# Performance work log

Measured on AMD Instinct MI355X. Metric: run time of the kernel, lower is better.

Reference implementation:

```python
import jax, jax.numpy as jnp
import numpy as np


def setup_inputs() -> dict:
    key = jax.random.key(0)
    k1, k2, k3, k4, k5 = jax.random.split(key, 5)
    B, C, H, W = 8, 256, 64, 64
    Cp = C // 8  # query/key channels
    x = jax.random.normal(k1, (B, C, H, W), dtype=jnp.float32)
    # 1x1 conv weights (bias=False in the module), spectral norm treated as a fixed weight scale
    Wq = jax.random.normal(k2, (Cp, C), dtype=jnp.float32) * 0.05
    Wk = jax.random.normal(k3, (Cp, C), dtype=jnp.float32) * 0.05
    Wv = jax.random.normal(k4, (C, C), dtype=jnp.float32) * 0.05
    gamma = jax.random.normal(k5, (1,), dtype=jnp.float32)
    return {"x": x, "Wq": Wq, "Wk": Wk, "Wv": Wv, "gamma": gamma}


def reference(x, Wq, Wk, Wv, gamma):
    B, C, H, W = x.shape
    xf = x.reshape(B, C, H * W)  # (B, C, N)
    # ConvLayer = 1x1 conv (no bias) followed by ReLU
    f = jax.nn.relu(jnp.einsum('oc,bcn->bon', Wq, xf))  # (B, C', N)
    g = jax.nn.relu(jnp.einsum('oc,bcn->bon', Wk, xf))  # (B, C', N)
    h = jax.nn.relu(jnp.einsum('oc,bcn->bon', Wv, xf))  # (B, C, N)
    # beta = softmax(f^T g, dim=1): normalize over the FIRST N axis (faithful to source)
    scores = jnp.einsum('bcn,bcm->bnm', f, g)  # (B, N, N)
    beta = jax.nn.softmax(scores, axis=1)
    o = gamma * jnp.einsum('bcn,bnm->bcm', h, beta) + xf  # (B, C, N)
    return o.reshape(B, C, H, W)
```

## Files before the change

kernel.cpp:

```cpp
#include <hip/hip_runtime.h>


typedef __attribute__((ext_vector_type(8))) short bf16x8;
typedef __attribute__((ext_vector_type(4))) float f32x4;
typedef __attribute__((ext_vector_type(4))) unsigned short us4;

#define LOG2E 1.44269504088896f

static __device__ __forceinline__ unsigned short f2bf(float x) {
    union { float f; unsigned u; } v; v.f = x;
    unsigned r = v.u + 0x7FFFu + ((v.u >> 16) & 1u);
    return (unsigned short)(r >> 16);
}
static __device__ __forceinline__ float bf2f(unsigned short u) {
    union { unsigned u; float f; } v; v.u = ((unsigned)u) << 16;
    return v.f;
}

__global__ __launch_bounds__(256) void wconv_kernel(
    const float* __restrict__ Wq, const float* __restrict__ Wk,
    const float* __restrict__ Wv, unsigned short* __restrict__ wq,
    unsigned short* __restrict__ wk, unsigned short* __restrict__ wv)
{
    const int i = blockIdx.x * 256 + threadIdx.x;
    if (i < 8192)            wq[i] = f2bf(Wq[i] * LOG2E);
    else if (i < 16384)      wk[i - 8192] = f2bf(Wk[i - 8192]);
    else                     wv[i - 16384] = f2bf(Wv[i - 16384]);
}

#define XPITCH 264
#define HPITCH 72
__global__ __launch_bounds__(256, 2) void producer_kernel(
    const float* __restrict__ x, const unsigned short* __restrict__ wq,
    const unsigned short* __restrict__ wk, const unsigned short* __restrict__ wv,
    unsigned short* __restrict__ f_t, unsigned short* __restrict__ g_t,
    unsigned short* __restrict__ h_bf, float* __restrict__ normg,
    float* __restrict__ pmax)
{
    __shared__ unsigned short xh_s[256 * HPITCH];
    __shared__ unsigned short fg_s[4 * 2 * 512];

    const int tid  = threadIdx.x;
    const int w    = tid >> 6;
    const int lane = tid & 63;
    const int q    = lane >> 4;
    const int r    = lane & 15;
    const int b    = blockIdx.x & 7;
    const int nt   = blockIdx.x >> 3;
    const int n0   = nt << 6;
    const size_t bN = (size_t)b << 12;
    const f32x4 zero = {0.f, 0.f, 0.f, 0.f};

#pragma unroll
    for (int jj = 0; jj < 4; jj++) {
        const int task = jj * 256 + tid;
        const int n4 = task & 15;
        const int c4 = task >> 4;
        float va[4][4];
#pragma unroll
        for (int i = 0; i < 4; i++) {
            const f32x4 v = __builtin_nontemporal_load(
                (const f32x4*)(x + ((size_t)b << 20)
                               + (size_t)(c4 * 4 + i) * 4096 + n0) + n4);
            va[i][0] = v.x; va[i][1] = v.y; va[i][2] = v.z; va[i][3] = v.w;
        }
#pragma unroll
        for (int i = 0; i < 4; i++) {
            us4 t;
            t.x = f2bf(va[0][i]); t.y = f2bf(va[1][i]);
            t.z = f2bf(va[2][i]); t.w = f2bf(va[3][i]);
            *(us4*)(xh_s + (n4 * 4 + i) * XPITCH + c4 * 4) = t;
        }
    }
    __syncthreads();

    f32x4 acch[4][4];
    f32x4 accf[2], accg[2];
#pragma unroll
    for (int cs = 0; cs < 4; cs++)
#pragma unroll
        for (int ns = 0; ns < 4; ns++) acch[cs][ns] = zero;
    accf[0] = accf[1] = accg[0] = accg[1] = zero;

    for (int ks = 0; ks < 8; ks++) {
        const int kof = ks * 32 + q * 8;
        bf16x8 av[4], aq[2], ak[2];
#pragma unroll
        for (int cs = 0; cs < 4; cs++)
            av[cs] = *(const bf16x8*)(wv + (size_t)(w * 64 + cs * 16 + r) * 256 + kof);
#pragma unroll
        for (int ms = 0; ms < 2; ms++) {
            aq[ms] = *(const bf16x8*)(wq + (size_t)(ms * 16 + r) * 256 + kof);
            ak[ms] = *(const bf16x8*)(wk + (size_t)(ms * 16 + r) * 256 + kof);
        }
#pragma unroll
        for (int ns = 0; ns < 4; ns++) {
            const bf16x8 bx = *(const bf16x8*)(xh_s + (ns * 16 + r) * XPITCH + kof);
#pragma unroll
            for (int cs = 0; cs < 4; cs++)
                acch[cs][ns] = __builtin_amdgcn_mfma_f32_16x16x32_bf16(av[cs], bx, acch[cs][ns], 0, 0, 0);
            if (ns == w) {
#pragma unroll
                for (int ms = 0; ms < 2; ms++) {
                    accf[ms] = __builtin_amdgcn_mfma_f32_16x16x32_bf16(aq[ms], bx, accf[ms], 0, 0, 0);
                    accg[ms] = __builtin_amdgcn_mfma_f32_16x16x32_bf16(ak[ms], bx, accg[ms], 0, 0, 0);
                }
            }
        }
    }

    unsigned short* lf = fg_s + w * 1024;
    unsigned short* lg = lf + 512;
#pragma unroll
    for (int ms = 0; ms < 2; ms++)
#pragma unroll
        for (int reg = 0; reg < 4; reg++) {
            lf[r * 32 + ms * 16 + q * 4 + reg] = f2bf(fmaxf(accf[ms][reg], 0.f));
            lg[r * 32 + ms * 16 + q * 4 + reg] = f2bf(fmaxf(accg[ms][reg], 0.f));
        }
    const bf16x8 ffrag = *(const bf16x8*)(lf + r * 32 + q * 8);
    const bf16x8 gfrag = *(const bf16x8*)(lg + r * 32 + q * 8);
    *(bf16x8*)(f_t + ((bN + n0 + w * 16 + r) << 5) + q * 8) = ffrag;
    *(bf16x8*)(g_t + ((bN + n0 + w * 16 + r) << 5) + q * 8) = gfrag;

    float nf2 = 0.f, ng2 = 0.f;
#pragma unroll
    for (int i = 0; i < 8; i++) {
        const float fv = bf2f(((unsigned short*)&ffrag)[i]);
        const float gv = bf2f(((unsigned short*)&gfrag)[i]);
        nf2 += fv * fv; ng2 += gv * gv;
    }
    nf2 += __shfl_xor(nf2, 16); nf2 += __shfl_xor(nf2, 32);
    ng2 += __shfl_xor(ng2, 16); ng2 += __shfl_xor(ng2, 32);
    if (q == 0) normg[bN + n0 + w * 16 + r] = sqrtf(ng2);
    float nf = sqrtf(nf2);
#pragma unroll
    for (int off = 1; off < 16; off <<= 1) nf = fmaxf(nf, __shfl_xor(nf, off));
    if (lane == 0) pmax[(b << 8) + nt * 4 + w] = nf;

    __syncthreads();
#pragma unroll
    for (int cs = 0; cs < 4; cs++)
#pragma unroll
        for (int ns = 0; ns < 4; ns++)
#pragma unroll
            for (int reg = 0; reg < 4; reg++)
                xh_s[(w * 64 + cs * 16 + q * 4 + reg) * HPITCH + ns * 16 + r] =
                    f2bf(fmaxf(acch[cs][ns][reg], 0.f));
    __syncthreads();
    const size_t hdst = ((size_t)(b * 64 + nt)) << 14;
#pragma unroll
    for (int p = 0; p < 8; p++) {
        const int c = p * 32 + (tid >> 3);
        const int k = tid & 7;
        *(bf16x8*)(h_bf + hdst + c * 64 + k * 8) =
            *(const bf16x8*)(xh_s + c * HPITCH + k * 8);
    }
}

__global__ __launch_bounds__(512, 4) void attn_kernel(
    const unsigned short* __restrict__ f_t, const unsigned short* __restrict__ g_t,
    const unsigned short* __restrict__ h_bf, const float* __restrict__ x,
    const float* __restrict__ gamma, const float* __restrict__ normg,
    const float* __restrict__ pmax, float* __restrict__ out)
{
    __shared__ unsigned short p_s[3][64 * 128];
    __shared__ float red_l[8][64];
    __shared__ float sLi[64];

    const int tid  = threadIdx.x;
    const int w    = tid >> 6;
    const int lane = tid & 63;
    const int q    = lane >> 4;
    const int r    = lane & 15;
    const int b    = blockIdx.x & 7;
    const int m0   = (blockIdx.x >> 3) << 6;

    const size_t bN = (size_t)b << 12;
    const int c0 = w << 5;

    float pv = pmax[(b << 8) + lane];
    pv = fmaxf(pv, pmax[(b << 8) + 64 + lane]);
    pv = fmaxf(pv, pmax[(b << 8) + 128 + lane]);
    pv = fmaxf(pv, pmax[(b << 8) + 192 + lane]);
#pragma unroll
    for (int off = 1; off < 64; off <<= 1) pv = fmaxf(pv, __shfl_xor(pv, off));
    const float mnf = pv;

    bf16x8 bg[4];
    float nMh[4];
#pragma unroll
    for (int ms = 0; ms < 4; ms++) {
        bg[ms] = *(const bf16x8*)(g_t + ((bN + m0 + ms * 16 + r) << 5) + (q << 3));
        nMh[ms] = -(mnf * normg[bN + m0 + ms * 16 + r] * 1.0002f);
    }

    f32x4 acc[2][4];
    const f32x4 zero = {0.f, 0.f, 0.f, 0.f};
#pragma unroll
    for (int cs = 0; cs < 2; cs++)
#pragma unroll
        for (int ms = 0; ms < 4; ms++) acc[cs][ms] = zero;
    float lt[4] = {0.f, 0.f, 0.f, 0.f};

    const int wchunk = (w << 1) + (q >> 1);
    const int wphys  = (wchunk & 8) | ((wchunk ^ r) & 7);
    const int woff   = (wphys << 3) + ((q & 1) << 2);

    auto ldf = [&](int t) {
        return *(const bf16x8*)(f_t + ((bN + (t << 7) + (w << 4) + r) << 5) + (q << 3));
    };
    auto produce = [&](const bf16x8 af, unsigned short* pb) {
#pragma unroll
        for (int ms = 0; ms < 4; ms++) {
            f32x4 ci; ci[0] = ci[1] = ci[2] = ci[3] = nMh[ms];
            const f32x4 sv = __builtin_amdgcn_mfma_f32_16x16x32_bf16(af, bg[ms], ci, 0, 0, 0);
            const float e0 = __builtin_amdgcn_exp2f(sv[0]);
            const float e1 = __builtin_amdgcn_exp2f(sv[1]);
            const float e2 = __builtin_amdgcn_exp2f(sv[2]);
            const float e3 = __builtin_amdgcn_exp2f(sv[3]);
            lt[ms] += (e0 + e1) + (e2 + e3);
            uint2 pk;
            pk.x = __builtin_amdgcn_perm(__float_as_uint(e1), __float_as_uint(e0), 0x07060302u);
            pk.y = __builtin_amdgcn_perm(__float_as_uint(e3), __float_as_uint(e2), 0x07060302u);
            *(uint2*)(pb + ((ms * 16 + r) << 7) + woff) = pk;
        }
    };

    bf16x8 afn = ldf(0);
    produce(afn, p_s[0]);
    afn = ldf(1);

    int sr = 0, sw = 1;
    for (int t = 0; t < 32; t++) {
        __syncthreads();
        bf16x8 ah[2][4];
#pragma unroll
        for (int ch = 0; ch < 4; ch++) {
            const unsigned short* hb =
                h_bf + (((size_t)(b * 64 + t * 2 + (ch >> 1))) << 14) + ((ch & 1) << 5) + (q << 3);
#pragma unroll
            for (int cs = 0; cs < 2; cs++)
                ah[cs][ch] = *(const bf16x8*)(hb + ((c0 + cs * 16 + r) << 6));
        }
        if (t < 31) {
            const bf16x8 afc = afn;
            if (t < 30) afn = ldf(t + 2);
            produce(afc, p_s[sw]);
        }
        const unsigned short* pb = p_s[sr];
#pragma unroll
        for (int ch = 0; ch < 4; ch++) {
            bf16x8 bp[4];
#pragma unroll
            for (int ms = 0; ms < 4; ms++) {
                const int idx  = (ch << 2) + q;
                const int phys = (idx & 8) | ((idx ^ r) & 7);
                bp[ms] = *(const bf16x8*)(pb + ((ms * 16 + r) << 7) + (phys << 3));
            }
#pragma unroll
            for (int cs = 0; cs < 2; cs++)
#pragma unroll
                for (int ms = 0; ms < 4; ms++)
                    acc[cs][ms] = __builtin_amdgcn_mfma_f32_16x16x32_bf16(
                        ah[cs][ch], bp[ms], acc[cs][ms], 0, 0, 0);
        }
        sr = sw;
        sw = (sw == 2) ? 0 : sw + 1;
    }

#pragma unroll
    for (int ms = 0; ms < 4; ms++) {
        lt[ms] += __shfl_xor(lt[ms], 16);
        lt[ms] += __shfl_xor(lt[ms], 32);
    }
    __syncthreads();
    if (q == 0)
#pragma unroll
        for (int ms = 0; ms < 4; ms++) red_l[w][ms * 16 + r] = lt[ms];
    __syncthreads();
    if (tid < 64) {
        float L = 0.f;
#pragma unroll
        for (int ww = 0; ww < 8; ww++) L += red_l[ww][tid];
        sLi[tid] = 1.f / L;
    }
    __syncthreads();

    const float gm = gamma[0];
#pragma unroll
    for (int cs = 0; cs < 2; cs++) {
#pragma unroll
        for (int ms = 0; ms < 4; ms++) {
            const float gl = gm * sLi[ms * 16 + r];
#pragma unroll
            for (int reg = 0; reg < 4; reg++) {
                const int c = c0 + cs * 16 + q * 4 + reg;
                const size_t a = (((size_t)b * 256 + c) << 12) + m0 + ms * 16 + r;
                const float xv = __builtin_nontemporal_load(x + a);
                __builtin_nontemporal_store(gl * acc[cs][ms][reg] + xv, out + a);
            }
        }
    }
}

extern "C" void kernel_launch(void* const* d_in, const int* in_sizes, int n_in,
                              void* d_out, int out_size, void* d_ws, size_t ws_size,
                              hipStream_t stream) {
    const float* x     = (const float*)d_in[0];
    const float* Wq    = (const float*)d_in[1];
    const float* Wk    = (const float*)d_in[2];
    const float* Wv    = (const float*)d_in[3];
    const float* gamma = (const float*)d_in[4];
    float* out = (float*)d_out;

    char* ws = (char*)d_ws;
    unsigned short* f_t  = (unsigned short*)ws;
    unsigned short* g_t  = (unsigned short*)(ws + (2u << 20));
    unsigned short* h_bf = (unsigned short*)(ws + (4u << 20));
    float*          ng   = (float*)(ws + (20u << 20));
    float*          pmx  = (float*)(ws + (20u << 20) + (1u << 17));
    unsigned short* wq   = (unsigned short*)(ws + (21u << 20));
    unsigned short* wk   = wq + 8192;
    unsigned short* wv   = wk + 8192;

    wconv_kernel<<<dim3(320), 256, 0, stream>>>(Wq, Wk, Wv, wq, wk, wv);
    producer_kernel<<<dim3(512), 256, 0, stream>>>(x, wq, wk, wv, f_t, g_t, h_bf, ng, pmx);
    attn_kernel<<<dim3(512), 512, 0, stream>>>(f_t, g_t, h_bf, x, gamma, ng, pmx, out);
}
```

Measured before the change: 251.0 us.

## Split producer h-projection into two passes with per-wave staging, raise MFMA priority

The producer kernel now computes the value projection in two passes of 32 channels per wave instead of all 64 at once. This halves the h accumulator registers and shrinks shared memory by giving x and the h staging buffer separate, smaller regions. Each wave writes its h tile through a private staging area, which removes the block-wide syncs before the h store. The attention kernel also wraps its MFMA block in s_setprio to favour matrix issue over other waves. The cost is reloading the x fragments from LDS twice, plus some extra loop overhead.

```diff
diff --git a/kernel.cpp b/kernel.cpp
--- a/kernel.cpp
+++ b/kernel.cpp
@@ -29,7 +29,7 @@
 }
 
 #define XPITCH 264
-#define HPITCH 72
+#define HSPITCH 72
 __global__ __launch_bounds__(256, 2) void producer_kernel(
     const float* __restrict__ x, const unsigned short* __restrict__ wq,
     const unsigned short* __restrict__ wk, const unsigned short* __restrict__ wv,
@@ -37,7 +37,8 @@
     unsigned short* __restrict__ h_bf, float* __restrict__ normg,
     float* __restrict__ pmax)
 {
-    __shared__ unsigned short xh_s[256 * HPITCH];
+    __shared__ unsigned short xh_s[64 * XPITCH];
+    __shared__ unsigned short hst[4 * 32 * HSPITCH];
     __shared__ unsigned short fg_s[4 * 2 * 512];
 
     const int tid  = threadIdx.x;
@@ -74,87 +75,91 @@
     }
     __syncthreads();
 
-    f32x4 acch[4][4];
     f32x4 accf[2], accg[2];
-#pragma unroll
-    for (int cs = 0; cs < 4; cs++)
-#pragma unroll
-        for (int ns = 0; ns < 4; ns++) acch[cs][ns] = zero;
     accf[0] = accf[1] = accg[0] = accg[1] = zero;
 
-    for (int ks = 0; ks < 8; ks++) {
-        const int kof = ks * 32 + q * 8;
-        bf16x8 av[4], aq[2], ak[2];
-#pragma unroll
-        for (int cs = 0; cs < 4; cs++)
-            av[cs] = *(const bf16x8*)(wv + (size_t)(w * 64 + cs * 16 + r) * 256 + kof);
-#pragma unroll
-        for (int ms = 0; ms < 2; ms++) {
-            aq[ms] = *(const bf16x8*)(wq + (size_t)(ms * 16 + r) * 256 + kof);
-            ak[ms] = *(const bf16x8*)(wk + (size_t)(ms * 16 + r) * 256 + kof);
-        }
-#pragma unroll
-        for (int ns = 0; ns < 4; ns++) {
-            const bf16x8 bx = *(const bf16x8*)(xh_s + (ns * 16 + r) * XPITCH + kof);
-#pragma unroll
-            for (int cs = 0; cs < 4; cs++)
-                acch[cs][ns] = __builtin_amdgcn_mfma_f32_16x16x32_bf16(av[cs], bx, acch[cs][ns], 0, 0, 0);
-            if (ns == w) {
-#pragma unroll
-                for (int ms = 0; ms < 2; ms++) {
-                    accf[ms] = __builtin_amdgcn_mfma_f32_16x16x32_bf16(aq[ms], bx, accf[ms], 0, 0, 0);
-                    accg[ms] = __builtin_amdgcn_mfma_f32_16x16x32_bf16(ak[ms], bx, accg[ms], 0, 0, 0);
+#pragma unroll
+    for (int pass = 0; pass < 2; pass++) {
+        f32x4 acch[2][4];
+#pragma unroll
+        for (int cs = 0; cs < 2; cs++)
+#pragma unroll
+            for (int ns = 0; ns < 4; ns++) acch[cs][ns] = zero;
+
+        for (int ks = 0; ks < 8; ks++) {
+            const int kof = ks * 32 + q * 8;
+            bf16x8 av0 = *(const bf16x8*)(wv + (size_t)(w * 64 + pass * 32 + r) * 256 + kof);
+            bf16x8 av1 = *(const bf16x8*)(wv + (size_t)(w * 64 + pass * 32 + 16 + r) * 256 + kof);
+            bf16x8 aq0, aq1, ak0, ak1;
+            if (pass == 0) {
+                aq0 = *(const bf16x8*)(wq + (size_t)(r) * 256 + kof);
+                aq1 = *(const bf16x8*)(wq + (size_t)(16 + r) * 256 + kof);
+                ak0 = *(const bf16x8*)(wk + (size_t)(r) * 256 + kof);
+                ak1 = *(const bf16x8*)(wk + (size_t)(16 + r) * 256 + kof);
+            }
+#pragma unroll
+            for (int ns = 0; ns < 4; ns++) {
+                const bf16x8 bx = *(const bf16x8*)(xh_s + (ns * 16 + r) * XPITCH + kof);
+                acch[0][ns] = __builtin_amdgcn_mfma_f32_16x16x32_bf16(av0, bx, acch[0][ns], 0, 0, 0);
+                acch[1][ns] = __builtin_amdgcn_mfma_f32_16x16x32_bf16(av1, bx, acch[1][ns], 0, 0, 0);
+                if (pass == 0 && ns == w) {
+                    accf[0] = __builtin_amdgcn_mfma_f32_16x16x32_bf16(aq0, bx, accf[0], 0, 0, 0);
+                    accf[1] = __builtin_amdgcn_mfma_f32_16x16x32_bf16(aq1, bx, accf[1], 0, 0, 0);
+                    accg[0] = __builtin_amdgcn_mfma_f32_16x16x32_bf16(ak0, bx, accg[0], 0, 0, 0);
+                    accg[1] = __builtin_amdgcn_mfma_f32_16x16x32_bf16(ak1, bx, accg[1], 0, 0, 0);
                 }
             }
         }
-    }
-
-    unsigned short* lf = fg_s + w * 1024;
-    unsigned short* lg = lf + 512;
-#pragma unroll
-    for (int ms = 0; ms < 2; ms++)
-#pragma unroll
-        for (int reg = 0; reg < 4; reg++) {
-            lf[r * 32 + ms * 16 + q * 4 + reg] = f2bf(fmaxf(accf[ms][reg], 0.f));
-            lg[r * 32 + ms * 16 + q * 4 + reg] = f2bf(fmaxf(accg[ms][reg], 0.f));
-        }
-    const bf16x8 ffrag = *(const bf16x8*)(lf + r * 32 + q * 8);
-    const bf16x8 gfrag = *(const bf16x8*)(lg + r * 32 + q * 8);
-    *(bf16x8*)(f_t + ((bN + n0 + w * 16 + r) << 5) + q * 8) = ffrag;
-    *(bf16x8*)(g_t + ((bN + n0 + w * 16 + r) << 5) + q * 8) = gfrag;
-
-    float nf2 = 0.f, ng2 = 0.f;
-#pragma unroll
-    for (int i = 0; i < 8; i++) {
-        const float fv = bf2f(((unsigned short*)&ffrag)[i]);
-        const float gv = bf2f(((unsigned short*)&gfrag)[i]);
-        nf2 += fv * fv; ng2 += gv * gv;
-    }
-    nf2 += __shfl_xor(nf2, 16); nf2 += __shfl_xor(nf2, 32);
-    ng2 += __shfl_xor(ng2, 16); ng2 += __shfl_xor(ng2, 32);
-    if (q == 0) normg[bN + n0 + w * 16 + r] = sqrtf(ng2);
-    float nf = sqrtf(nf2);
-#pragma unroll
-    for (int off = 1; off < 16; off <<= 1) nf = fmaxf(nf, __shfl_xor(nf, off));
-    if (lane == 0) pmax[(b << 8) + nt * 4 + w] = nf;
-
-    __syncthreads();
-#pragma unroll
-    for (int cs = 0; cs < 4; cs++)
-#pragma unroll
-        for (int ns = 0; ns < 4; ns++)
-#pragma unroll
-            for (int reg = 0; reg < 4; reg++)
-                xh_s[(w * 64 + cs * 16 + q * 4 + reg) * HPITCH + ns * 16 + r] =
-                    f2bf(fmaxf(acch[cs][ns][reg], 0.f));
-    __syncthreads();
-    const size_t hdst = ((size_t)(b * 64 + nt)) << 14;
-#pragma unroll
-    for (int p = 0; p < 8; p++) {
-        const int c = p * 32 + (tid >> 3);
-        const int k = tid & 7;
-        *(bf16x8*)(h_bf + hdst + c * 64 + k * 8) =
-            *(const bf16x8*)(xh_s + c * HPITCH + k * 8);
+
+        if (pass == 0) {
+            unsigned short* lf = fg_s + w * 1024;
+            unsigned short* lg = lf + 512;
+#pragma unroll
+            for (int ms = 0; ms < 2; ms++)
+#pragma unroll
+                for (int reg = 0; reg < 4; reg++) {
+                    lf[r * 32 + ms * 16 + q * 4 + reg] = f2bf(fmaxf(accf[ms][reg], 0.f));
+                    lg[r * 32 + ms * 16 + q * 4 + reg] = f2bf(fmaxf(accg[ms][reg], 0.f));
+                }
+            const bf16x8 ffrag = *(const bf16x8*)(lf + r * 32 + q * 8);
+            const bf16x8 gfrag = *(const bf16x8*)(lg + r * 32 + q * 8);
+            *(bf16x8*)(f_t + ((bN + n0 + w * 16 + r) << 5) + q * 8) = ffrag;
+            *(bf16x8*)(g_t + ((bN + n0 + w * 16 + r) << 5) + q * 8) = gfrag;
+
+            float nf2 = 0.f, ng2 = 0.f;
+#pragma unroll
+            for (int i = 0; i < 8; i++) {
+                const float fv = bf2f(((unsigned short*)&ffrag)[i]);
+                const float gv = bf2f(((unsigned short*)&gfrag)[i]);
+                nf2 += fv * fv; ng2 += gv * gv;
+            }
+            nf2 += __shfl_xor(nf2, 16); nf2 += __shfl_xor(nf2, 32);
+            ng2 += __shfl_xor(ng2, 16); ng2 += __shfl_xor(ng2, 32);
+            if (q == 0) normg[bN + n0 + w * 16 + r] = sqrtf(ng2);
+            float nf = sqrtf(nf2);
+#pragma unroll
+            for (int off = 1; off < 16; off <<= 1) nf = fmaxf(nf, __shfl_xor(nf, off));
+            if (lane == 0) pmax[(b << 8) + nt * 4 + w] = nf;
+        }
+
+        unsigned short* hs = hst + w * (32 * HSPITCH);
+#pragma unroll
+        for (int cs = 0; cs < 2; cs++)
+#pragma unroll
+            for (int ns = 0; ns < 4; ns++)
+#pragma unroll
+                for (int reg = 0; reg < 4; reg++)
+                    hs[(cs * 16 + q * 4 + reg) * HSPITCH + ns * 16 + r] =
+                        f2bf(fmaxf(acch[cs][ns][reg], 0.f));
+        const size_t hdst = (((size_t)(b * 64 + nt)) << 14)
+                          + (size_t)(w * 64 + pass * 32) * 64;
+#pragma unroll
+        for (int p = 0; p < 4; p++) {
+            const int cl = p * 8 + (lane >> 3);
+            const int kk = lane & 7;
+            *(bf16x8*)(h_bf + hdst + cl * 64 + kk * 8) =
+                *(const bf16x8*)(hs + cl * HSPITCH + kk * 8);
+        }
     }
 }
 
@@ -258,12 +263,14 @@
                 const int phys = (idx & 8) | ((idx ^ r) & 7);
                 bp[ms] = *(const bf16x8*)(pb + ((ms * 16 + r) << 7) + (phys << 3));
             }
+            __builtin_amdgcn_s_setprio(1);
 #pragma unroll
             for (int cs = 0; cs < 2; cs++)
 #pragma unroll
                 for (int ms = 0; ms < 4; ms++)
                     acc[cs][ms] = __builtin_amdgcn_mfma_f32_16x16x32_bf16(
                         ah[cs][ch], bp[ms], acc[cs][ms], 0, 0, 0);
+            __builtin_amdgcn_s_setprio(0);
         }
         sr = sw;
         sw = (sw == 2) ? 0 : sw + 1;
```

Result: slower. 288.0 us (+14.7%).
